# Kernel tuning notes

Measured on AMD Instinct MI355X. Metric: run time of the kernel, lower is better.

## Reference

```python
import jax, jax.numpy as jnp
import numpy as np

NUM_HEADS = 8

def conv1x1(w, x, b=None):
    # w: [O, C], x: [B, C, H, W] -> [B, O, H, W]
    y = jnp.einsum('oc,bchw->bohw', w, x)
    if b is not None:
        y = y + b[None, :, None, None]
    return y

def setup_inputs() -> dict:
    key = jax.random.key(0)
    ks = jax.random.split(key, 8)
    B, C, H, W = 8, 512, 32, 32
    s = lambda fan: 1.0 / np.sqrt(fan)
    return {
        'x': jax.random.normal(ks[0], (B, C, H, W), jnp.float32),
        'W_qkv': jax.random.normal(ks[1], (3 * C, C), jnp.float32) * s(C),
        'W_proj': jax.random.normal(ks[2], (C, C), jnp.float32) * s(C),
        'b_proj': jax.random.normal(ks[3], (C,), jnp.float32) * 0.01,
        'W_att1': jax.random.normal(ks[4], (C // 4, C), jnp.float32) * s(C),
        'b_att1': jax.random.normal(ks[5], (C // 4,), jnp.float32) * 0.01,
        'W_att2': jax.random.normal(ks[6], (1, C // 4), jnp.float32) * s(C // 4),
        'b_att2': jax.random.normal(ks[7], (1,), jnp.float32) * 0.01,
    }

def reference(x, W_qkv, W_proj, b_proj, W_att1, b_att1, W_att2, b_att2):
    B, C, H, W = x.shape
    nh = NUM_HEADS
    dh = C // nh
    N = H * W
    qkv = conv1x1(W_qkv, x)                      # [B, 3C, H, W]
    qkv = qkv.reshape(B, 3, nh, dh, N)
    qkv = jnp.transpose(qkv, (1, 0, 2, 4, 3))    # [3, B, nh, N, dh]
    q, k, v = qkv[0], qkv[1], qkv[2]
    attn = jnp.einsum('bhnd,bhmd->bhnm', q, k) * (dh ** -0.5)
    attn = jax.nn.softmax(attn, axis=-1)         # dropout is identity at eval
    o = jnp.einsum('bhnm,bhmd->bhnd', attn, v)   # [B, nh, N, dh]
    # Faithful to torch: transpose(1,2) then raw reshape to (B, C, H, W)
    o = jnp.swapaxes(o, 1, 2).reshape(B, C, H, W)
    out = conv1x1(W_proj, o, b_proj)             # [B, C, H, W]
    h1 = jax.nn.relu(conv1x1(W_att1, out, b_att1))
    spatial_att = jax.nn.sigmoid(conv1x1(W_att2, h1, b_att2))  # [B, 1, H, W]
    out = out * spatial_att
    return (out, spatial_att)
```

## Files before the change

### kernel.cpp

```cpp
#include <hip/hip_runtime.h>
#include <hip/hip_bf16.h>

using bf16 = __hip_bfloat16;
typedef __bf16 bf16x8 __attribute__((ext_vector_type(8)));
typedef float  f32x4  __attribute__((ext_vector_type(4)));


static constexpr int B  = 8;
static constexpr int C  = 512;
static constexpr int N  = 1024;
static constexpr int NH = 8;
static constexpr int DH = 64;
static constexpr int CQ = 128;

static constexpr float QSCALE = 0.125f * 1.44269504f;

static constexpr size_t QKV_OFF  = 0;
static constexpr size_t H1_OFF   = 25165824;

__device__ __forceinline__ unsigned pack2(float lo, float hi) {
  __hip_bfloat162 h = __float22bfloat162_rn(make_float2(lo, hi));
  return *(unsigned*)&h;
}
__device__ __forceinline__ int swz(int row, int col) {
  return row * 64 + ((((col >> 3) ^ row) & 7) << 3) + (col & 7);
}
__device__ __forceinline__ bf16x8 ldfrag(const short* tl, int row, int kk, int lane) {
  const int atom = 4 * kk + (lane >> 4);
  return *(const bf16x8*)&tl[row * 64 + (((atom ^ row) & 7) << 3)];
}
__device__ __forceinline__ bf16x8 ldfragF(const short* tl, int row, int kk, int lane) {
  const int atom = 4 * kk + (lane >> 4);
  return *(const bf16x8*)&tl[row * 64 + (((atom ^ row ^ (row >> 2)) & 7) << 3)];
}
__device__ __forceinline__ int fswz(int row, int col) {
  return row * 64 + ((((col >> 2) ^ row) & 15) << 2) + (col & 3);
}
__device__ __forceinline__ void swap32(unsigned &a, unsigned &b) {
  asm("v_permlane32_swap_b32 %0, %1" : "+v"(a), "+v"(b));
}
__device__ __forceinline__ void swap16(unsigned &a, unsigned &b) {
  asm("v_permlane16_swap_b32 %0, %1" : "+v"(a), "+v"(b));
}

__global__ __launch_bounds__(256, 3) void k_qkv(const float* __restrict__ W,
                                                const float* __restrict__ x,
                                                bf16* __restrict__ qkv) {
  __shared__ __align__(16) short Al[128 * 64];
  __shared__ __align__(16) short Bl[128 * 64];
  const int pt = blockIdx.x, ot = blockIdx.y, b = blockIdx.z;
  const int p0 = pt * 128, o0 = ot * 128;
  const int t = threadIdx.x, l = t & 63, w = t >> 6;
  const int wo = w & 1, wp = w >> 1;
  const int g = t >> 5, k32 = t & 31;
  const int r16 = t >> 4, q16 = t & 15;
  const float* xsrc = x + ((size_t)b * C + 8 * g) * N + p0 + 4 * k32;
  const float* wsrc = W + (size_t)(o0 + r16) * C + 4 * q16;
  unsigned upx[16], upw[16];
  auto ld = [&](int kc) {
    const float* xa = xsrc + (size_t)kc * N;
#pragma unroll
    for (int u = 0; u < 4; ++u) {
      float4 r0 = *(const float4*)(xa + (size_t)(2 * u) * N);
      float4 r1 = *(const float4*)(xa + (size_t)(2 * u + 1) * N);
      upx[4*u+0] = pack2(r0.x, r1.x);
      upx[4*u+1] = pack2(r0.y, r1.y);
      upx[4*u+2] = pack2(r0.z, r1.z);
      upx[4*u+3] = pack2(r0.w, r1.w);
    }
    const float* wa = wsrc + kc;
#pragma unroll
    for (int i = 0; i < 8; ++i) {
      float4 f = *(const float4*)(wa + (size_t)(16 * i) * C);
      upw[2*i]   = pack2(f.x, f.y);
      upw[2*i+1] = pack2(f.z, f.w);
    }
  };
  f32x4 acc[4][4] = {};
  ld(0);
  for (int kc = 0; kc < C; kc += 64) {
    __syncthreads();
#pragma unroll
    for (int j = 0; j < 4; ++j) {
      const int p = 4 * k32 + j;
      uint4 v = make_uint4(upx[j], upx[4 + j], upx[8 + j], upx[12 + j]);
      *(uint4*)&Al[p * 64 + (((g ^ p ^ (p >> 2)) & 7) << 3)] = v;
    }
#pragma unroll
    for (int i = 0; i < 8; ++i) {
      const int R = 16 * i + r16;
      *(uint2*)&Bl[R * 64 + ((((q16 >> 1) ^ R) & 7) << 3) + 4 * (q16 & 1)] =
          make_uint2(upw[2 * i], upw[2 * i + 1]);
    }
    __syncthreads();
    if (kc + 64 < C) ld(kc + 64);
#pragma unroll
    for (int kk = 0; kk < 2; ++kk) {
      bf16x8 af[4], bf[4];
#pragma unroll
      for (int i = 0; i < 4; ++i) af[i] = ldfrag(Bl, wo*64 + i*16 + (l&15), kk, l);
#pragma unroll
      for (int j = 0; j < 4; ++j) bf[j] = ldfragF(Al, wp*64 + j*16 + (l&15), kk, l);
#pragma unroll
      for (int i = 0; i < 4; ++i)
#pragma unroll
        for (int j = 0; j < 4; ++j)
          acc[i][j] = __builtin_amdgcn_mfma_f32_16x16x32_bf16(af[i], bf[j], acc[i][j], 0, 0, 0);
    }
  }
  const float qs = (ot < 4) ? QSCALE : 1.0f;
  __syncthreads();
  {
    short* T = wo ? Bl : Al;
#pragma unroll
    for (int i = 0; i < 4; ++i) {
      const int d = i * 16 + 4 * (l >> 4);
#pragma unroll
      for (int j = 0; j < 4; ++j) {
        const int p = wp * 64 + j * 16 + (l & 15);
        *(unsigned*)&T[swz(p, d)]     = pack2(acc[i][j][0] * qs, acc[i][j][1] * qs);
        *(unsigned*)&T[swz(p, d + 2)] = pack2(acc[i][j][2] * qs, acc[i][j][3] * qs);
      }
    }
  }
  __syncthreads();
  {
    const int oc0 = o0, oc1 = o0 + 64;
    bf16* dst0 = qkv + (size_t)(oc0 >> 9) * (B * NH * N * DH) +
                 (size_t)(b * NH + ((oc0 >> 6) & 7)) * N * DH + (size_t)p0 * DH;
    bf16* dst1 = qkv + (size_t)(oc1 >> 9) * (B * NH * N * DH) +
                 (size_t)(b * NH + ((oc1 >> 6) & 7)) * N * DH + (size_t)p0 * DH;
#pragma unroll
    for (int it = 0; it < 8; ++it) {
      const int e = t + 256 * it;
      const int tile = e >> 10, row = (e >> 3) & 127, atom = e & 7;
      const short* T = tile ? Bl : Al;
      uint4 val = *(const uint4*)&T[row * 64 + (((atom ^ row) & 7) << 3)];
      bf16* dst = tile ? dst1 : dst0;
      *(uint4*)(dst + (size_t)row * DH + atom * 8) = val;
    }
  }
}

__global__ __launch_bounds__(256) void k_attn(bf16* __restrict__ qkv) {
  __shared__ __align__(16) short Ql[64 * 64];
  __shared__ __align__(16) short Kl[64 * 64];
  __shared__ __align__(16) short Vt[64 * 64];
  __shared__ __align__(16) short Pb[4 * 16 * 64];
  const int bh = blockIdx.x, qt = blockIdx.y;
  const int t = threadIdx.x, l = t & 63, w = t >> 6;
  const bf16* kp = qkv + (size_t)B * NH * N * DH;
  const bf16* vp = kp + (size_t)B * NH * N * DH;
  const uint4* gkb = (const uint4*)(kp + (size_t)bh * N * DH);
  const uint4* gvb = (const uint4*)(vp + (size_t)bh * N * DH);
  const int kpr = t & 31, g = t >> 5;

  {
    const uint4* gq = (const uint4*)(qkv + ((size_t)bh * N + qt * 64) * DH);
    for (int c = t; c < 512; c += 256) {
      int row = c >> 3, atom = c & 7;
      *(uint4*)&Ql[row * 64 + (((atom ^ row) & 7) << 3)] = gq[c];
    }
  }
  __syncthreads();
  bf16x8 qf[2] = { ldfrag(Ql, w * 16 + (l & 15), 0, l),
                   ldfrag(Ql, w * 16 + (l & 15), 1, l) };
  f32x4 oacc[4] = {};
  f32x4 lacc = {};
  short* Pw = &Pb[w * 1024];

  bf16x8 onesf;
#pragma unroll
  for (int i = 0; i < 8; ++i) onesf[i] = (__bf16)1.0f;

  uint4 kreg0, kreg1, v0, v1;
  auto ld = [&](int mt) {
    const uint4* gk = gkb + mt * 512;
    kreg0 = gk[t]; kreg1 = gk[t + 256];
    const uint4* gv = gvb + mt * 512;
    v0 = gv[16 * kpr + g]; v1 = gv[16 * kpr + 8 + g];
  };
  ld(0);

  for (int mt = 0; mt < 16; ++mt) {
    __syncthreads();
    {
      const int r0 = t >> 3, a0 = t & 7;
      *(uint4*)&Kl[r0 * 64 + (((a0 ^ r0) & 7) << 3)] = kreg0;
      const int r1 = r0 + 32;
      *(uint4*)&Kl[r1 * 64 + (((a0 ^ r1) & 7) << 3)] = kreg1;
      const unsigned* v0d = (const unsigned*)&v0;
      const unsigned* v1d = (const unsigned*)&v1;
#pragma unroll
      for (int j = 0; j < 8; ++j) {
        unsigned pk = __builtin_amdgcn_perm(v1d[j >> 1], v0d[j >> 1],
                                            (j & 1) ? 0x07060302u : 0x05040100u);
        *(unsigned*)&Vt[swz(g * 8 + j, 2 * kpr)] = pk;
      }
    }
    __syncthreads();
    if (mt < 15) ld(mt + 1);
    f32x4 sacc[4] = {};
#pragma unroll
    for (int kk = 0; kk < 2; ++kk)
#pragma unroll
      for (int kt = 0; kt < 4; ++kt) {
        bf16x8 af = ldfrag(Kl, kt * 16 + (l & 15), kk, l);
        sacc[kt] = __builtin_amdgcn_mfma_f32_16x16x32_bf16(af, qf[kk], sacc[kt], 0, 0, 0);
      }
    unsigned D[4][2];
#pragma unroll
    for (int kt = 0; kt < 4; ++kt) {
      float p0v = __builtin_exp2f(sacc[kt][0]);
      float p1v = __builtin_exp2f(sacc[kt][1]);
      float p2v = __builtin_exp2f(sacc[kt][2]);
      float p3v = __builtin_exp2f(sacc[kt][3]);
      D[kt][0] = pack2(p0v, p1v);
      D[kt][1] = pack2(p2v, p3v);
    }
#pragma unroll
    for (int kk = 0; kk < 2; ++kk) {
      unsigned a0 = D[2*kk][0], b0 = D[2*kk + 1][0];
      unsigned a1 = D[2*kk][1], b1 = D[2*kk + 1][1];
      swap32(a0, b0); swap16(a0, b0);
      swap32(a1, b1); swap16(a1, b1);
      uint4 pv = make_uint4(a0, a1, b0, b1);
      bf16x8 pbf = *(bf16x8*)&pv;
      lacc = __builtin_amdgcn_mfma_f32_16x16x32_bf16(onesf, pbf, lacc, 0, 0, 0);
#pragma unroll
      for (int dt = 0; dt < 4; ++dt) {
        bf16x8 av = ldfrag(Vt, dt * 16 + (l & 15), kk, l);
        oacc[dt] = __builtin_amdgcn_mfma_f32_16x16x32_bf16(av, pbf, oacc[dt], 0, 0, 0);
      }
    }
  }
  __syncthreads();
  const float inv = 1.f / lacc[0];
  const int qr = l & 15, cb0 = 4 * (l >> 4);
#pragma unroll
  for (int dt = 0; dt < 4; ++dt) {
    const int cb = dt * 16 + cb0;
    *(unsigned*)&Pw[swz(qr, cb)]     = pack2(oacc[dt][0] * inv, oacc[dt][1] * inv);
    *(unsigned*)&Pw[swz(qr, cb + 2)] = pack2(oacc[dt][2] * inv, oacc[dt][3] * inv);
  }
  __syncthreads();
  bf16* obase = qkv + ((size_t)bh * N + qt * 64 + w * 16) * DH;
#pragma unroll
  for (int i = 0; i < 2; ++i) {
    const int e = l + 64 * i, row = e >> 3, atom = e & 7;
    uint4 val = *(const uint4*)&Pw[row * 64 + (((atom ^ row) & 7) << 3)];
    *(uint4*)(obase + (size_t)row * DH + atom * 8) = val;
  }
}

__global__ __launch_bounds__(256) void k_proj(const float* __restrict__ Wp,
                                              const float* __restrict__ bp,
                                              const bf16* __restrict__ obuf,
                                              float* __restrict__ outd) {
  __shared__ __align__(16) short SM[8192];
  short* Wl = SM;
  short* Ot = SM + 4096;
  const int pt = blockIdx.x, ct = blockIdx.y, b = blockIdx.z;
  const int p0 = pt * 64, co0 = ct * 64;
  const int h = (p0 & 511) >> 6, eps = p0 >> 9;
  const int t = threadIdx.x, l = t & 63, w = t >> 6;
  const int r16 = t >> 4, q16 = t & 15;
  const int jp = t >> 3, a8 = t & 7;
  const float* wsrc = &Wp[(size_t)(co0 + r16) * C + 4 * q16];
  const bf16* obase = obuf + (size_t)(b * NH + h) * N * DH;
  float4 wreg[4]; uint4 or0, or1;
  auto ld = [&](int kc) {
    const float* wa = wsrc + kc;
#pragma unroll
    for (int i = 0; i < 4; ++i)
      wreg[i] = *(const float4*)(wa + (size_t)(16 * i) * C);
    const bf16* ob = obase + (size_t)(2 * (kc + 2 * jp) + eps) * 64 + 8 * a8;
    or0 = *(const uint4*)(ob);
    or1 = *(const uint4*)(ob + 128);
  };
  f32x4 acc[4] = {};
  ld(0);
  for (int kc = 0; kc < C; kc += 64) {
    __syncthreads();
#pragma unroll
    for (int i = 0; i < 4; ++i) {
      const int R = 16 * i + r16;
      *(uint2*)&Wl[R * 64 + ((((q16 >> 1) ^ R) & 7) << 3) + 4 * (q16 & 1)] =
          make_uint2(pack2(wreg[i].x, wreg[i].y), pack2(wreg[i].z, wreg[i].w));
    }
    {
      const unsigned* o0d = (const unsigned*)&or0;
      const unsigned* o1d = (const unsigned*)&or1;
#pragma unroll
      for (int dd = 0; dd < 8; ++dd) {
        unsigned pk = __builtin_amdgcn_perm(o1d[dd >> 1], o0d[dd >> 1],
                                            (dd & 1) ? 0x07060302u : 0x05040100u);
        const int row = 8 * a8 + dd;
        *(unsigned*)&Ot[row * 64 + ((((jp >> 2) ^ row ^ (row >> 2)) & 7) << 3) +
                        ((2 * jp) & 7)] = pk;
      }
    }
    __syncthreads();
    if (kc + 64 < C) ld(kc + 64);
    const int mrow = w * 16 + (l & 15);
#pragma unroll
    for (int kk = 0; kk < 2; ++kk) {
      bf16x8 a = ldfragF(Ot, mrow, kk, l);
#pragma unroll
      for (int nt = 0; nt < 4; ++nt) {
        bf16x8 bf = ldfrag(Wl, nt * 16 + (l & 15), kk, l);
        acc[nt] = __builtin_amdgcn_mfma_f32_16x16x32_bf16(a, bf, acc[nt], 0, 0, 0);
      }
    }
  }
  __syncthreads();
  {
    float* Ep = (float*)SM;
    const int pp = w * 16 + 4 * (l >> 4);
#pragma unroll
    for (int nt = 0; nt < 4; ++nt) {
      const int co = nt * 16 + (l & 15);
      const float bias = bp[co0 + co];
      *(float2*)&Ep[fswz(co, pp)]     = make_float2(acc[nt][0] + bias, acc[nt][1] + bias);
      *(float2*)&Ep[fswz(co, pp + 2)] = make_float2(acc[nt][2] + bias, acc[nt][3] + bias);
    }
  }
  __syncthreads();
  {
    const float* Ep = (const float*)SM;
#pragma unroll
    for (int it = 0; it < 4; ++it) {
      const int e = t + 256 * it;
      const int co = e >> 4, a = e & 15;
      float4 v = *(const float4*)&Ep[co * 64 + (((a ^ (co & 15)) & 15) << 2)];
      *(float4*)&outd[(size_t)b * C * N + (size_t)(co0 + co) * N + p0 + a * 4] = v;
    }
  }
}

__global__ __launch_bounds__(256) void k_att1(const float* __restrict__ W1,
                                              const float* __restrict__ b1,
                                              const float* __restrict__ outd,
                                              bf16* __restrict__ h1b) {
  __shared__ __align__(16) short Wl[64 * 64];
  __shared__ __align__(16) short Xt[64 * 64];
  const int pt = blockIdx.x, jt = blockIdx.y, b = blockIdx.z;
  const int p0 = pt * 64, j0 = jt * 64;
  const int t = threadIdx.x, l = t & 63, w = t >> 6;
  const int r16 = t >> 4, q16 = t & 15;
  const float* wsrc = &W1[(size_t)(j0 + r16) * C + 4 * q16];
  const float* xb = &outd[(size_t)b * C * N + p0 + 4 * q16];
  float4 wreg[4], xr[4];
  auto ld = [&](int kc) {
    const float* wa = wsrc + kc;
#pragma unroll
    for (int i = 0; i < 4; ++i)
      wreg[i] = *(const float4*)(wa + (size_t)(16 * i) * C);
#pragma unroll
    for (int i = 0; i < 4; ++i)
      xr[i] = *(const float4*)(xb + (size_t)(kc + 4 * r16 + i) * N);
  };
  f32x4 acc[4] = {};
  ld(0);
  for (int kc = 0; kc < C; kc += 64) {
    __syncthreads();
#pragma unroll
    for (int i = 0; i < 4; ++i) {
      const int R = 16 * i + r16;
      *(uint2*)&Wl[R * 64 + ((((q16 >> 1) ^ R) & 7) << 3) + 4 * (q16 & 1)] =
          make_uint2(pack2(wreg[i].x, wreg[i].y), pack2(wreg[i].z, wreg[i].w));
    }
    {
      const float* x0 = (const float*)&xr[0];
      const float* x1 = (const float*)&xr[1];
      const float* x2 = (const float*)&xr[2];
      const float* x3 = (const float*)&xr[3];
#pragma unroll
      for (int dd = 0; dd < 4; ++dd) {
        unsigned lo = pack2(x0[dd], x1[dd]);
        unsigned hi = pack2(x2[dd], x3[dd]);
        const int row = 4 * q16 + dd;
        *(uint2*)&Xt[row * 64 + ((((r16 >> 1) ^ row ^ (row >> 2)) & 7) << 3) +
                     ((4 * r16) & 7)] = make_uint2(lo, hi);
      }
    }
    __syncthreads();
    if (kc + 64 < C) ld(kc + 64);
    const int mrow = w * 16 + (l & 15);
#pragma unroll
    for (int kk = 0; kk < 2; ++kk) {
      bf16x8 a = ldfragF(Xt, mrow, kk, l);
#pragma unroll
      for (int nt = 0; nt < 4; ++nt) {
        bf16x8 bf = ldfrag(Wl, nt * 16 + (l & 15), kk, l);
        acc[nt] = __builtin_amdgcn_mfma_f32_16x16x32_bf16(a, bf, acc[nt], 0, 0, 0);
      }
    }
  }
  __syncthreads();
  {
    const int pp = w * 16 + 4 * (l >> 4);
#pragma unroll
    for (int nt = 0; nt < 4; ++nt) {
      const int jo = nt * 16 + (l & 15);
      const float bias = b1[j0 + jo];
      float v0 = fmaxf(acc[nt][0] + bias, 0.f), v1 = fmaxf(acc[nt][1] + bias, 0.f);
      float v2 = fmaxf(acc[nt][2] + bias, 0.f), v3 = fmaxf(acc[nt][3] + bias, 0.f);
      *(unsigned*)&Wl[swz(jo, pp)]     = pack2(v0, v1);
      *(unsigned*)&Wl[swz(jo, pp + 2)] = pack2(v2, v3);
    }
  }
  __syncthreads();
#pragma unroll
  for (int it = 0; it < 2; ++it) {
    const int e = t + 256 * it;
    const int row = e >> 3, atom = e & 7;
    uint4 val = *(const uint4*)&Wl[row * 64 + (((atom ^ row) & 7) << 3)];
    *(uint4*)((bf16*)h1b + (size_t)b * CQ * N + (size_t)(j0 + row) * N + p0 + atom * 8) = val;
  }
}

__global__ __launch_bounds__(256) void k_gate(const float* __restrict__ W2,
                                              const float* __restrict__ b2,
                                              const bf16* __restrict__ h1b,
                                              float* __restrict__ out0,
                                              float* __restrict__ out1) {
  __shared__ float red[8][32];
  __shared__ __align__(16) float att[32];
  const int blk = blockIdx.x, t = threadIdx.x;
  const int b = blk >> 5, p0 = (blk & 31) * 32;
  const int pl = t & 31, jg = t >> 5;
  float acc = 0.f;
  const bf16* hb = h1b + ((size_t)b * CQ + jg * 16) * N + p0 + pl;
#pragma unroll
  for (int jj = 0; jj < 16; ++jj)
    acc += W2[jg * 16 + jj] * __bfloat162float(hb[(size_t)jj * N]);
  red[jg][pl] = acc;
  __syncthreads();
  if (t < 32) {
    float a = b2[0];
#pragma unroll
    for (int k = 0; k < 8; ++k) a += red[k][t];
    const float sg = 1.f / (1.f + __expf(-a));
    att[t] = sg;
    out1[b * N + p0 + t] = sg;
  }
  __syncthreads();
  const int p4 = t & 7, cc = t >> 3;
  float4* ob4 = (float4*)(out0 + (size_t)b * C * N + p0);
  const float4 sg4 = *(const float4*)&att[4 * p4];
  for (int c = cc; c < C; c += 32) {
    float4 v = ob4[c * 256 + p4];
    v.x *= sg4.x; v.y *= sg4.y; v.z *= sg4.z; v.w *= sg4.w;
    ob4[c * 256 + p4] = v;
  }
}

extern "C" void kernel_launch(void* const* d_in, const int* in_sizes, int n_in,
                              void* d_out, int out_size, void* d_ws, size_t ws_size,
                              hipStream_t stream) {
  const float* x     = (const float*)d_in[0];
  const float* Wqkv  = (const float*)d_in[1];
  const float* Wproj = (const float*)d_in[2];
  const float* bproj = (const float*)d_in[3];
  const float* Watt1 = (const float*)d_in[4];
  const float* batt1 = (const float*)d_in[5];
  const float* Watt2 = (const float*)d_in[6];
  const float* batt2 = (const float*)d_in[7];

  char* ws = (char*)d_ws;
  bf16* qkvb = (bf16*)(ws + QKV_OFF);
  bf16* h1b  = (bf16*)(ws + H1_OFF);

  float* out0 = (float*)d_out;
  float* out1 = out0 + (size_t)B * C * N;

  k_qkv <<<dim3(8, 12, 8), 256, 0, stream>>>(Wqkv, x, qkvb);
  k_attn<<<dim3(64, 16),   256, 0, stream>>>(qkvb);
  k_proj<<<dim3(16, 8, 8), 256, 0, stream>>>(Wproj, bproj, qkvb, out0);
  k_att1<<<dim3(16, 2, 8), 256, 0, stream>>>(Watt1, batt1, out0, h1b);
  k_gate<<<256, 256, 0, stream>>>(Watt2, batt2, h1b, out0, out1);
}
```

Measured before the change: 172.5 us.

## Split QKV GEMM block into 512 threads with separate x and W loader roles

The QKV projection kernel now runs 512 threads per block instead of 256. Half the threads load and convert x while the other half load W, and each wave computes a 64x32 output sub-tile instead of 64x64. This halves per-thread accumulator and staging registers and adds more waves to hide global-load latency. In exchange, each wave reads the shared-memory A fragments more times relative to the MFMA work it does, and the larger block synchronises more threads at each barrier.

```diff
diff --git a/kernel.cpp b/kernel.cpp
--- a/kernel.cpp
+++ b/kernel.cpp
@@ -43,7 +43,7 @@
   asm("v_permlane16_swap_b32 %0, %1" : "+v"(a), "+v"(b));
 }
 
-__global__ __launch_bounds__(256, 3) void k_qkv(const float* __restrict__ W,
+__global__ __launch_bounds__(512, 6) void k_qkv(const float* __restrict__ W,
                                                 const float* __restrict__ x,
                                                 bf16* __restrict__ qkv) {
   __shared__ __align__(16) short Al[128 * 64];
@@ -52,59 +52,67 @@
   const int p0 = pt * 128, o0 = ot * 128;
   const int t = threadIdx.x, l = t & 63, w = t >> 6;
   const int wo = w & 1, wp = w >> 1;
-  const int g = t >> 5, k32 = t & 31;
-  const int r16 = t >> 4, q16 = t & 15;
+  const bool xrole = (t < 256);
+  const int g = (t >> 5) & 7, k32 = t & 31;
+  const int tu = t & 255;
+  const int r16 = tu >> 4, q16 = tu & 15;
   const float* xsrc = x + ((size_t)b * C + 8 * g) * N + p0 + 4 * k32;
   const float* wsrc = W + (size_t)(o0 + r16) * C + 4 * q16;
-  unsigned upx[16], upw[16];
+  unsigned up[16];
   auto ld = [&](int kc) {
-    const float* xa = xsrc + (size_t)kc * N;
-#pragma unroll
-    for (int u = 0; u < 4; ++u) {
-      float4 r0 = *(const float4*)(xa + (size_t)(2 * u) * N);
-      float4 r1 = *(const float4*)(xa + (size_t)(2 * u + 1) * N);
-      upx[4*u+0] = pack2(r0.x, r1.x);
-      upx[4*u+1] = pack2(r0.y, r1.y);
-      upx[4*u+2] = pack2(r0.z, r1.z);
-      upx[4*u+3] = pack2(r0.w, r1.w);
-    }
-    const float* wa = wsrc + kc;
-#pragma unroll
-    for (int i = 0; i < 8; ++i) {
-      float4 f = *(const float4*)(wa + (size_t)(16 * i) * C);
-      upw[2*i]   = pack2(f.x, f.y);
-      upw[2*i+1] = pack2(f.z, f.w);
+    if (xrole) {
+      const float* xa = xsrc + (size_t)kc * N;
+#pragma unroll
+      for (int u = 0; u < 4; ++u) {
+        float4 r0 = *(const float4*)(xa + (size_t)(2 * u) * N);
+        float4 r1 = *(const float4*)(xa + (size_t)(2 * u + 1) * N);
+        up[4*u+0] = pack2(r0.x, r1.x);
+        up[4*u+1] = pack2(r0.y, r1.y);
+        up[4*u+2] = pack2(r0.z, r1.z);
+        up[4*u+3] = pack2(r0.w, r1.w);
+      }
+    } else {
+      const float* wa = wsrc + kc;
+#pragma unroll
+      for (int i = 0; i < 8; ++i) {
+        float4 f = *(const float4*)(wa + (size_t)(16 * i) * C);
+        up[2*i]   = pack2(f.x, f.y);
+        up[2*i+1] = pack2(f.z, f.w);
+      }
     }
   };
-  f32x4 acc[4][4] = {};
+  f32x4 acc[4][2] = {};
   ld(0);
   for (int kc = 0; kc < C; kc += 64) {
     __syncthreads();
-#pragma unroll
-    for (int j = 0; j < 4; ++j) {
-      const int p = 4 * k32 + j;
-      uint4 v = make_uint4(upx[j], upx[4 + j], upx[8 + j], upx[12 + j]);
-      *(uint4*)&Al[p * 64 + (((g ^ p ^ (p >> 2)) & 7) << 3)] = v;
-    }
-#pragma unroll
-    for (int i = 0; i < 8; ++i) {
-      const int R = 16 * i + r16;
-      *(uint2*)&Bl[R * 64 + ((((q16 >> 1) ^ R) & 7) << 3) + 4 * (q16 & 1)] =
-          make_uint2(upw[2 * i], upw[2 * i + 1]);
+    if (xrole) {
+#pragma unroll
+      for (int j = 0; j < 4; ++j) {
+        const int p = 4 * k32 + j;
+        uint4 v = make_uint4(up[j], up[4 + j], up[8 + j], up[12 + j]);
+        *(uint4*)&Al[p * 64 + (((g ^ p ^ (p >> 2)) & 7) << 3)] = v;
+      }
+    } else {
+#pragma unroll
+      for (int i = 0; i < 8; ++i) {
+        const int R = 16 * i + r16;
+        *(uint2*)&Bl[R * 64 + ((((q16 >> 1) ^ R) & 7) << 3) + 4 * (q16 & 1)] =
+            make_uint2(up[2 * i], up[2 * i + 1]);
+      }
     }
     __syncthreads();
     if (kc + 64 < C) ld(kc + 64);
 #pragma unroll
     for (int kk = 0; kk < 2; ++kk) {
-      bf16x8 af[4], bf[4];
+      bf16x8 af[4], bf[2];
 #pragma unroll
       for (int i = 0; i < 4; ++i) af[i] = ldfrag(Bl, wo*64 + i*16 + (l&15), kk, l);
 #pragma unroll
-      for (int j = 0; j < 4; ++j) bf[j] = ldfragF(Al, wp*64 + j*16 + (l&15), kk, l);
+      for (int j = 0; j < 2; ++j) bf[j] = ldfragF(Al, wp*32 + j*16 + (l&15), kk, l);
 #pragma unroll
       for (int i = 0; i < 4; ++i)
 #pragma unroll
-        for (int j = 0; j < 4; ++j)
+        for (int j = 0; j < 2; ++j)
           acc[i][j] = __builtin_amdgcn_mfma_f32_16x16x32_bf16(af[i], bf[j], acc[i][j], 0, 0, 0);
     }
   }
@@ -116,8 +124,8 @@
     for (int i = 0; i < 4; ++i) {
       const int d = i * 16 + 4 * (l >> 4);
 #pragma unroll
-      for (int j = 0; j < 4; ++j) {
-        const int p = wp * 64 + j * 16 + (l & 15);
+      for (int j = 0; j < 2; ++j) {
+        const int p = wp * 32 + j * 16 + (l & 15);
         *(unsigned*)&T[swz(p, d)]     = pack2(acc[i][j][0] * qs, acc[i][j][1] * qs);
         *(unsigned*)&T[swz(p, d + 2)] = pack2(acc[i][j][2] * qs, acc[i][j][3] * qs);
       }
@@ -131,8 +139,8 @@
     bf16* dst1 = qkv + (size_t)(oc1 >> 9) * (B * NH * N * DH) +
                  (size_t)(b * NH + ((oc1 >> 6) & 7)) * N * DH + (size_t)p0 * DH;
 #pragma unroll
-    for (int it = 0; it < 8; ++it) {
-      const int e = t + 256 * it;
+    for (int it = 0; it < 4; ++it) {
+      const int e = t + 512 * it;
       const int tile = e >> 10, row = (e >> 3) & 127, atom = e & 7;
       const short* T = tile ? Bl : Al;
       uint4 val = *(const uint4*)&T[row * 64 + (((atom ^ row) & 7) << 3)];
@@ -475,7 +483,7 @@
   float* out0 = (float*)d_out;
   float* out1 = out0 + (size_t)B * C * N;
 
-  k_qkv <<<dim3(8, 12, 8), 256, 0, stream>>>(Wqkv, x, qkvb);
+  k_qkv <<<dim3(8, 12, 8), 512, 0, stream>>>(Wqkv, x, qkvb);
   k_attn<<<dim3(64, 16),   256, 0, stream>>>(qkvb);
   k_proj<<<dim3(16, 8, 8), 256, 0, stream>>>(Wproj, bproj, qkvb, out0);
   k_att1<<<dim3(16, 2, 8), 256, 0, stream>>>(Watt1, batt1, out0, h1b);
```

Result: slower. 181.3 us (+5.1%).
